# Kernel optimization log

Hardware: AMD Instinct MI355X
Metric: run time of the kernel (lower is better)

## Reference

```python
import jax, jax.numpy as jnp
import numpy as np

B, D, E, H, TOP_K = 8192, 1024, 16, 1024, 8
LOSS_COEF = 0.01
NOISE_EPS = 0.01
INV_SQRT2 = 0.7071067811865476


def _normal_cdf(z):
    return 0.5 * (1.0 + jax.lax.erf(z * INV_SQRT2))


def _cv_squared(v):
    v = v.astype(jnp.float32)
    return jnp.var(v, ddof=1) / (jnp.mean(v) ** 2 + 1e-10)


def setup_inputs() -> dict:
    key = jax.random.key(0)
    k1, k2, k3, k4, k5, k6 = jax.random.split(key, 6)
    return {
        "x": jax.random.normal(k1, (B, D), dtype=jnp.float32),
        "w_gate": jax.random.normal(k2, (D, E), dtype=jnp.float32) * 0.02,
        "w_noise": jax.random.normal(k3, (D, E), dtype=jnp.float32) * 0.02,
        "expert_w": jax.random.normal(k4, (E, D, H), dtype=jnp.float32) * (1.0 / np.sqrt(D)),
        "expert_b": jax.random.normal(k5, (E, H), dtype=jnp.float32) * 0.01,
        "noise": jax.random.normal(k6, (B, E), dtype=jnp.float32),
    }


def reference(x, w_gate, w_noise, expert_w, expert_b, noise):
    # ---- noisy top-k gating (training=True) ----
    clean_logits = x @ w_gate                                   # [B, E]
    raw_noise_stddev = x @ w_noise                              # [B, E]
    noise_stddev = jax.nn.softplus(raw_noise_stddev) + NOISE_EPS
    noisy_logits = clean_logits + noise * noise_stddev          # [B, E]
    probs = jax.nn.softmax(noisy_logits, axis=1)                # [B, E]

    m = min(TOP_K + 1, E)
    top_logits, top_indices = jax.lax.top_k(probs, m)           # [B, m]
    top_k_logits = top_logits[:, :TOP_K]
    top_k_indices = top_indices[:, :TOP_K]
    top_k_gates = top_k_logits / (jnp.sum(top_k_logits, axis=1, keepdims=True) + 1e-6)

    rows = jnp.arange(B)[:, None]
    gates = jnp.zeros_like(probs).at[rows, top_k_indices].set(top_k_gates)  # [B, E]

    # ---- prob-in-top-k load (top_k < num_experts, training) ----
    # faithful to source: thresholds come from softmaxed top values,
    # compared against pre-softmax noisy/clean logits (as in original code)
    threshold_if_in = top_logits[:, TOP_K][:, None]             # [B, 1]
    threshold_if_out = top_logits[:, TOP_K - 1][:, None]        # [B, 1]
    is_in = noisy_logits > threshold_if_in
    prob_if_in = _normal_cdf((clean_logits - threshold_if_in) / noise_stddev)
    prob_if_out = _normal_cdf((clean_logits - threshold_if_out) / noise_stddev)
    load = jnp.where(is_in, prob_if_in, prob_if_out).sum(axis=0)  # [E]

    importance = gates.sum(axis=0)                              # [E]
    loss = LOSS_COEF * (_cv_squared(importance) + _cv_squared(load))

    # ---- experts: per-expert linear, gate-weighted sum over experts ----
    # y[b,h] = sum_e gates[b,e] * (x[b,:] @ W[e] + b[e])[h]
    y = jnp.einsum('bd,edh,be->bh', x, expert_w, gates) + gates @ expert_b
    return y, loss
```

## Files before the change

### kernel.cpp

```cpp
#include <hip/hip_runtime.h>
#include <cstdint>

#define B_SZ 8192
#define D_SZ 1024
#define E_SZ 16
#define H_SZ 1024
#define MAXTILES 272

using short8 = __attribute__((ext_vector_type(8))) short;
using f32x4  = __attribute__((ext_vector_type(4))) float;

__device__ __forceinline__ unsigned short f2bf(float f) {
  union { float f; unsigned int u; } v; v.f = f;
  unsigned int u = v.u;
  return (unsigned short)((u + 0x7fffu + ((u >> 16) & 1u)) >> 16);
}
__device__ __forceinline__ float bf2f(unsigned short h) {
  union { unsigned int u; float f; } v; v.u = ((unsigned int)h) << 16; return v.f;
}

__device__ __forceinline__ void async_ld16(void* lds, const void* g) {
  __builtin_amdgcn_global_load_lds(
      reinterpret_cast<const unsigned int __attribute__((address_space(1)))*>(
          reinterpret_cast<uintptr_t>(g)),
      reinterpret_cast<unsigned int __attribute__((address_space(3)))*>(
          reinterpret_cast<uintptr_t>(lds)),
      16, 0, 0);
}

__global__ __launch_bounds__(256) void prep(
    const float* __restrict__ x, const float* __restrict__ wg,
    const float* __restrict__ wn, const float* __restrict__ ew,
    unsigned short* __restrict__ xb, unsigned short* __restrict__ wtb,
    float* __restrict__ cl, float* __restrict__ rn, float* __restrict__ stats) {
  __shared__ __align__(16) float psm[2 * 32 * 132];
  const int bx = blockIdx.x;
  const int tid = threadIdx.x;

  if (bx < 256) {
    float* sx  = psm;
    float* swT = psm + 32 * 132;
    const int lane = tid & 63;
    const int wave = tid >> 6;
    const int row  = lane & 31;
    const int half = lane >> 5;
    const int rowbase = bx * 32;
    float acc[8] = {0.f, 0.f, 0.f, 0.f, 0.f, 0.f, 0.f, 0.f};

    const int srow = tid >> 3;
    const int sd   = (tid & 7) * 16;
    const int wd   = tid >> 1;
    const int wc   = (tid & 1) * 16;
    const float* wsrc = (wc == 0) ? wg : wn;

    for (int ch = 0; ch < 8; ++ch) {
      __syncthreads();
      #pragma unroll
      for (int k = 0; k < 4; ++k) {
        const float4 v = *(const float4*)(
            x + (size_t)(rowbase + srow) * D_SZ + ch * 128 + sd + k * 4);
        *(float4*)&sx[srow * 132 + sd + k * 4] = v;
      }
      {
        const float* wp = wsrc + (size_t)(ch * 128 + wd) * 16;
        float wv[16];
        #pragma unroll
        for (int k = 0; k < 4; ++k)
          *(float4*)&wv[k * 4] = *(const float4*)(wp + k * 4);
        #pragma unroll
        for (int j = 0; j < 16; ++j) swT[(wc + j) * 132 + wd] = wv[j];
      }
      __syncthreads();
      #pragma unroll 4
      for (int dg = 0; dg < 16; ++dg) {
        const int d = half * 64 + dg * 4;
        const f32x4 xv = *(const f32x4*)&sx[row * 132 + d];
        #pragma unroll
        for (int c = 0; c < 8; ++c) {
          const f32x4 wv = *(const f32x4*)&swT[(wave * 8 + c) * 132 + d];
          acc[c] = fmaf(xv[0], wv[0], acc[c]);
          acc[c] = fmaf(xv[1], wv[1], acc[c]);
          acc[c] = fmaf(xv[2], wv[2], acc[c]);
          acc[c] = fmaf(xv[3], wv[3], acc[c]);
        }
      }
    }
    #pragma unroll
    for (int c = 0; c < 8; ++c) acc[c] += __shfl_down(acc[c], 32);
    if (lane < 32) {
      const int cg = wave * 8;
      float* dst = (cg < 16) ? (cl + (size_t)(rowbase + row) * 16 + cg)
                             : (rn + (size_t)(rowbase + row) * 16 + (cg - 16));
      *(float4*)dst = *(const float4*)&acc[0];
      *(float4*)(dst + 4) = *(const float4*)&acc[4];
    }
  } else if (bx < 4352) {
    const int b = bx - 256;
    const size_t i = (size_t)b * 256 + tid;
    const float4 v0 = ((const float4*)x)[2 * i];
    const float4 v1 = ((const float4*)x)[2 * i + 1];
    unsigned short r[8] = {f2bf(v0.x), f2bf(v0.y), f2bf(v0.z), f2bf(v0.w),
                           f2bf(v1.x), f2bf(v1.y), f2bf(v1.z), f2bf(v1.w)};
    ((short8*)xb)[i] = *(const short8*)r;
    if (b == 0 && tid < 48) stats[tid] = 0.0f;
  } else {
    float (*t)[65] = (float(*)[65])psm;
    const int b = bx - 4352;
    const int e  = b >> 8;
    const int d0 = ((b >> 4) & 15) * 64;
    const int h0 = (b & 15) * 64;
    const float* We = ew + (size_t)e * D_SZ * H_SZ;
    unsigned short* Wte = wtb + (size_t)e * D_SZ * H_SZ;
    #pragma unroll
    for (int i = 0; i < 4; ++i) {
      const int idx = i * 256 + tid;
      const int r = idx >> 4, co = (idx & 15) * 4;
      *(float4*)&t[r][co] =
          *(const float4*)(We + (size_t)(d0 + r) * H_SZ + h0 + co);
    }
    __syncthreads();
    #pragma unroll
    for (int i = 0; i < 2; ++i) {
      const int idx = i * 256 + tid;
      const int r = idx >> 3, c8 = (idx & 7) * 8;
      unsigned short v[8];
      #pragma unroll
      for (int j = 0; j < 8; ++j) v[j] = f2bf(t[c8 + j][r]);
      *(short8*)(Wte + (size_t)(h0 + r) * D_SZ + d0 + c8) = *(const short8*)v;
    }
  }
}

__global__ __launch_bounds__(64) void gating_post(
    const float* __restrict__ clg, const float* __restrict__ rng,
    const float* __restrict__ noise, float* __restrict__ gates,
    float* __restrict__ stats, int* __restrict__ rowidx, int* __restrict__ rowmap) {
  int* gcount = (int*)(stats + 32);
  __shared__ int lcnt[16];
  __shared__ int lbase[16];
  const int row = blockIdx.x * 64 + threadIdx.x;
  if (threadIdx.x < 16) lcnt[threadIdx.x] = 0;
  float cl[16], sd[16], nl[16], p[16];
  #pragma unroll
  for (int e = 0; e < 16; ++e) {
    cl[e] = clg[(size_t)row * 16 + e];
    const float r = rng[(size_t)row * 16 + e];
    sd[e] = fmaxf(r, 0.0f) + log1pf(expf(-fabsf(r))) + 0.01f;
    nl[e] = cl[e] + noise[(size_t)row * 16 + e] * sd[e];
  }
  float mx = nl[0];
  #pragma unroll
  for (int e = 1; e < 16; ++e) mx = fmaxf(mx, nl[e]);
  float sum = 0.0f;
  #pragma unroll
  for (int e = 0; e < 16; ++e) { p[e] = expf(nl[e] - mx); sum += p[e]; }
  const float inv = 1.0f / sum;
  #pragma unroll
  for (int e = 0; e < 16; ++e) p[e] *= inv;
  float tmp[16];
  #pragma unroll
  for (int e = 0; e < 16; ++e) tmp[e] = p[e];
  float tv[9]; int ti[9];
  for (int k = 0; k < 9; ++k) {
    float bv = tmp[0]; int bj = 0;
    #pragma unroll
    for (int j = 1; j < 16; ++j) if (tmp[j] > bv) { bv = tmp[j]; bj = j; }
    tv[k] = bv; ti[k] = bj; tmp[bj] = -1.0f;
  }
  float s8 = 0.0f;
  #pragma unroll
  for (int k = 0; k < 8; ++k) s8 += tv[k];
  const float denom = s8 + 1e-6f;
  float g[16];
  #pragma unroll
  for (int e = 0; e < 16; ++e) g[e] = 0.0f;
  for (int k = 0; k < 8; ++k) g[ti[k]] = tv[k] / denom;
  const float thr_in = tv[8], thr_out = tv[7];
  float lc[16];
  #pragma unroll
  for (int e = 0; e < 16; ++e) {
    const float t = (nl[e] > thr_in) ? thr_in : thr_out;
    lc[e] = 0.5f * (1.0f + erff(((cl[e] - t) / sd[e]) * 0.70710678118654752f));
  }
  #pragma unroll
  for (int e = 0; e < 16; ++e) gates[(size_t)row * 16 + e] = g[e];
  __syncthreads();
  int myslot[8];
  #pragma unroll
  for (int k = 0; k < 8; ++k) myslot[k] = atomicAdd(&lcnt[ti[k]], 1);
  __syncthreads();
  if (threadIdx.x < 16) lbase[threadIdx.x] = atomicAdd(&gcount[threadIdx.x], lcnt[threadIdx.x]);
  __syncthreads();
  #pragma unroll
  for (int k = 0; k < 8; ++k) {
    const int e = ti[k];
    const int slot = lbase[e] + myslot[k];
    rowidx[e * B_SZ + slot] = row;
    rowmap[row * 8 + k] = (e << 13) | slot;
  }
  #pragma unroll
  for (int e = 0; e < 16; ++e) {
    float vi = g[e], vl = lc[e];
    for (int o = 32; o > 0; o >>= 1) { vi += __shfl_down(vi, o); vl += __shfl_down(vl, o); }
    if (threadIdx.x == 0) {
      atomicAdd(&stats[e], vi);
      atomicAdd(&stats[16 + e], vl);
    }
  }
}

__global__ __launch_bounds__(512, 2) void moe_gemm(
    const unsigned short* __restrict__ Xb,
    const unsigned short* __restrict__ Wt,
    const float* __restrict__ gates,
    const float* __restrict__ ebias,
    const float* __restrict__ stats,
    const int* __restrict__ rowidx,
    unsigned short* __restrict__ partial) {
  __shared__ __align__(16) char smem[133120];
  int*   sRI = (int*)(smem + 131072);
  float* sGG = (float*)(smem + 132096);

  const int* gcount = (const int*)(stats + 32);
  int my_e = -1, tile = 0, tstart = 0, acc_t = 0;
  #pragma unroll
  for (int ee = 0; ee < 16; ++ee) {
    const int nt_e = (gcount[ee] + 255) >> 8;
    if (my_e < 0 && (int)blockIdx.y < acc_t + nt_e) {
      my_e = ee; tile = (int)blockIdx.y - acc_t; tstart = acc_t;
    }
    acc_t += nt_e;
  }
  if (my_e < 0) return;
  const int e = my_e;
  const int slot0 = tile << 8;
  const int cnt = gcount[e];
  const int col0 = (int)blockIdx.x << 8;

  const int tid  = (int)threadIdx.x;
  const int lane = tid & 63;
  const int wave = tid >> 6;
  const int wm = wave >> 2, wn = wave & 3;
  const int ml = lane & 15;
  const int quad = lane >> 4;
  const int wb = tid & ~63;

  if (tid < 256) {
    const int slot = slot0 + tid;
    const int ok = slot < cnt;
    const int row = ok ? rowidx[e * B_SZ + slot] : 0;
    sRI[tid] = row;
    sGG[tid] = ok ? gates[(size_t)row * 16 + e] : 0.0f;
  }
  __syncthreads();

  const int gc = (tid & 7) ^ ((tid >> 3) & 7);
  const int rl = tid >> 3;
  const unsigned short* const We = Wt + (size_t)e * D_SZ * H_SZ;
  const unsigned short* a_src0 = Xb + (size_t)sRI[rl]       * D_SZ + gc * 8;
  const unsigned short* a_src1 = Xb + (size_t)sRI[64 + rl]  * D_SZ + gc * 8;
  const unsigned short* a_src2 = Xb + (size_t)sRI[128 + rl] * D_SZ + gc * 8;
  const unsigned short* a_src3 = Xb + (size_t)sRI[192 + rl] * D_SZ + gc * 8;
  const unsigned short* b_src0 = We + (size_t)(col0 + rl)   * D_SZ + gc * 8;

#define STG_A(kt, l) \
  async_ld16(smem + (((kt) & 1) * 32768) + ((((l) * 512 + wb)) << 4), \
             a_src##l + (kt) * 64)
#define STG_B(kt, l) \
  async_ld16(smem + 65536 + (((kt) & 1) * 32768) + ((((l) * 512 + wb)) << 4), \
             b_src0 + (l) * 65536 + (kt) * 64)

  STG_A(0,0); STG_A(0,1);  STG_A(0,2); STG_A(0,3);
  STG_B(0,0); STG_B(0,1);  STG_B(0,2); STG_B(0,3);
  STG_A(1,0); STG_A(1,1);  STG_A(1,2); STG_A(1,3);
  STG_B(1,0); STG_B(1,1);
  asm volatile("s_waitcnt vmcnt(6)" ::: "memory");
  __builtin_amdgcn_s_barrier();

  f32x4 acc[8][4] = {};

#define MF16(I0) \
  do { __builtin_amdgcn_s_setprio(1); \
    _Pragma("unroll") for (int ii = 0; ii < 2; ++ii) \
      _Pragma("unroll") for (int j = 0; j < 4; ++j) \
        _Pragma("unroll") for (int kk = 0; kk < 2; ++kk) \
          acc[(I0)+ii][j] = __builtin_amdgcn_mfma_f32_16x16x32_bf16( \
              af[(I0)+ii][kk], bf[j][kk], acc[(I0)+ii][j], 0, 0, 0); \
    __builtin_amdgcn_s_setprio(0); } while (0)

  #pragma unroll
  for (int kt = 0; kt < 16; ++kt) {
    const unsigned short* sAb =
        (const unsigned short*)(smem + ((kt & 1) ? 32768 : 0));
    const unsigned short* sBb =
        (const unsigned short*)(smem + 65536 + ((kt & 1) ? 32768 : 0));
    if (kt + 1 < 16) { STG_B(kt+1,2); STG_B(kt+1,3); }
    short8 af[8][2], bf[4][2];
    #pragma unroll
    for (int i = 0; i < 8; ++i) {
      const int m = wm * 128 + i * 16 + ml;
      #pragma unroll
      for (int kk = 0; kk < 2; ++kk) {
        const int c = (kk * 4 + quad) ^ (m & 7);
        af[i][kk] = *(const short8*)(sAb + (size_t)(m * 8 + c) * 8);
      }
    }
    #pragma unroll
    for (int j = 0; j < 4; ++j) {
      const int n = wn * 64 + j * 16 + ml;
      #pragma unroll
      for (int kk = 0; kk < 2; ++kk) {
        const int c = (kk * 4 + quad) ^ (n & 7);
        bf[j][kk] = *(const short8*)(sBb + (size_t)(n * 8 + c) * 8);
      }
    }
    MF16(0);
    asm volatile("s_waitcnt lgkmcnt(0)" ::: "memory");
    __builtin_amdgcn_s_barrier();
    if (kt + 2 < 16) { STG_A(kt+2,0); STG_A(kt+2,1); }
    MF16(2);
    if (kt + 2 < 16) { STG_A(kt+2,2); STG_A(kt+2,3); }
    MF16(4);
    if (kt + 2 < 16) { STG_B(kt+2,0); STG_B(kt+2,1); }
    MF16(6);
    if (kt <= 13) {
      asm volatile("s_waitcnt vmcnt(6)" ::: "memory");
      __builtin_amdgcn_s_barrier();
    } else if (kt == 14) {
      asm volatile("s_waitcnt vmcnt(0)" ::: "memory");
      __builtin_amdgcn_s_barrier();
    }
  }
#undef MF16
#undef STG_A
#undef STG_B

  __syncthreads();
  float ebv[4];
  #pragma unroll
  for (int j = 0; j < 4; ++j)
    ebv[j] = ebias[(size_t)e * H_SZ + col0 + wn * 64 + j * 16 + ml];
  unsigned short* sOut = (unsigned short*)smem;
  const size_t prow0 = (size_t)((tstart << 8) + slot0);
  #pragma unroll
  for (int half = 0; half < 2; ++half) {
    if (wm == half) {
      #pragma unroll
      for (int i = 0; i < 8; ++i) {
        const int lr = i * 16 + quad * 4;
        #pragma unroll
        for (int r = 0; r < 4; ++r) {
          const float gv = sGG[half * 128 + lr + r];
          #pragma unroll
          for (int j = 0; j < 4; ++j) {
            const int cc = wn * 64 + j * 16 + ml;
            sOut[(lr + r) * 264 + cc] = f2bf(gv * (acc[i][j][r] + ebv[j]));
          }
        }
      }
    }
    __syncthreads();
    #pragma unroll
    for (int it = 0; it < 8; ++it) {
      const int s = it * 512 + tid;
      const int rr = s >> 5;
      const int c8 = (s & 31) * 8;
      const short8 v = *(const short8*)(sOut + rr * 264 + c8);
      __builtin_nontemporal_store(
          v, (short8*)(partial + (prow0 + half * 128 + rr) * H_SZ + col0 + c8));
    }
    __syncthreads();
  }
}

__global__ __launch_bounds__(256) void reduce_k(
    const unsigned short* __restrict__ partial, const int* __restrict__ rowmap,
    const float* __restrict__ stats, float* __restrict__ y) {
  const int row0 = blockIdx.x * 4;
  const int tid = threadIdx.x;
  const int* gcount = (const int*)(stats + 32);
  __shared__ int sp[4][8];
  if (tid < 32) {
    const int r = tid >> 3, k = tid & 7;
    const int v = rowmap[(row0 + r) * 8 + k];
    const int e = v >> 13, slot = v & 8191;
    int t = 0;
    #pragma unroll
    for (int ee = 0; ee < 16; ++ee) t += (ee < e) ? ((gcount[ee] + 255) >> 8) : 0;
    sp[r][k] = (t << 8) + slot;
  }
  __syncthreads();
  const int r = tid >> 6;
  const int c0 = (tid & 63) * 16;
  float a[16];
  #pragma unroll
  for (int j = 0; j < 16; ++j) a[j] = 0.f;
  #pragma unroll
  for (int k = 0; k < 8; ++k) {
    const unsigned short* pp = partial + (size_t)sp[r][k] * H_SZ + c0;
    const short8 p0 = *(const short8*)pp;
    const short8 p1 = *(const short8*)(pp + 8);
    #pragma unroll
    for (int j = 0; j < 8; ++j) {
      a[j]     += bf2f((unsigned short)p0[j]);
      a[j + 8] += bf2f((unsigned short)p1[j]);
    }
  }
  float* yp = y + (size_t)(row0 + r) * H_SZ + c0;
  #pragma unroll
  for (int q = 0; q < 4; ++q) {
    float4 o = {a[q * 4], a[q * 4 + 1], a[q * 4 + 2], a[q * 4 + 3]};
    *(float4*)(yp + q * 4) = o;
  }

  if (blockIdx.x == 0 && tid == 0) {
    double si = 0.0, sl = 0.0;
    for (int e = 0; e < 16; ++e) { si += stats[e]; sl += stats[16 + e]; }
    const double mi = si / 16.0, mld = sl / 16.0;
    double vi = 0.0, vl = 0.0;
    for (int e = 0; e < 16; ++e) {
      const double di = stats[e] - mi;       vi += di * di;
      const double dl = stats[16 + e] - mld; vl += dl * dl;
    }
    vi /= 15.0; vl /= 15.0;
    const double loss = 0.01 * (vi / (mi * mi + 1e-10) + vl / (mld * mld + 1e-10));
    y[(size_t)B_SZ * H_SZ] = (float)loss;
  }
}

extern "C" void kernel_launch(void* const* d_in, const int* in_sizes, int n_in,
                              void* d_out, int out_size, void* d_ws, size_t ws_size,
                              hipStream_t stream) {
  (void)in_sizes; (void)n_in; (void)out_size; (void)ws_size;
  const float* x    = (const float*)d_in[0];
  const float* wg   = (const float*)d_in[1];
  const float* wnoi = (const float*)d_in[2];
  const float* ew   = (const float*)d_in[3];
  const float* eb   = (const float*)d_in[4];
  const float* nz   = (const float*)d_in[5];
  float* y = (float*)d_out;

  char* ws = (char*)d_ws;
  const size_t MB = 1024 * 1024;
  unsigned short* xb     = (unsigned short*)(ws);
  unsigned short* wtb    = (unsigned short*)(ws + 16 * MB);
  float* cl              = (float*)(ws + 48 * MB);
  float* rn              = (float*)(ws + 48 * MB + 512 * 1024);
  float* gates           = (float*)(ws + 49 * MB);
  int*   rowidx          = (int*)  (ws + 49 * MB + 512 * 1024);
  int*   rowmap          = (int*)  (ws + 50 * MB);
  float* stats           = (float*)(ws + 50 * MB + 512 * 1024);
  unsigned short* partial= (unsigned short*)(ws + 52 * MB);

  hipLaunchKernelGGL(prep,        dim3(8448),         dim3(256), 0, stream,
                     x, wg, wnoi, ew, xb, wtb, cl, rn, stats);
  hipLaunchKernelGGL(gating_post, dim3(128),          dim3(64),  0, stream,
                     cl, rn, nz, gates, stats, rowidx, rowmap);
  hipLaunchKernelGGL(moe_gemm,    dim3(4, MAXTILES),  dim3(512), 0, stream,
                     xb, wtb, gates, eb, stats, rowidx, partial);
  hipLaunchKernelGGL(reduce_k,    dim3(2048),         dim3(256), 0, stream,
                     partial, rowmap, stats, y);
}
```

Baseline: 391.3 us.

## Interleave per-phase LDS reads with MFMA blocks and reorder async staging

Restructures the main K-loop of the expert GEMM into four phases. Each phase reads only a 2-row slice of A fragments from LDS, then waits and runs its MFMA block, rather than loading all A fragments up front. Global-to-LDS staging is reordered so that the A halves for the next tile and the B halves for tile+2 are issued between phases. The aim is to cut register pressure and overlap LDS reads with MFMAs, at the cost of many more barriers per iteration. The stage ordering also changes which buffers the vmcnt(6) waits cover, so correctness depends on the new issue order lining up with the waits.

```diff
diff --git a/kernel.cpp b/kernel.cpp
--- a/kernel.cpp
+++ b/kernel.cpp
@@ -270,22 +270,43 @@
   async_ld16(smem + 65536 + (((kt) & 1) * 32768) + ((((l) * 512 + wb)) << 4), \
              b_src0 + (l) * 65536 + (kt) * 64)
 
-  STG_A(0,0); STG_A(0,1);  STG_A(0,2); STG_A(0,3);
-  STG_B(0,0); STG_B(0,1);  STG_B(0,2); STG_B(0,3);
-  STG_A(1,0); STG_A(1,1);  STG_A(1,2); STG_A(1,3);
-  STG_B(1,0); STG_B(1,1);
+  STG_A(0,0); STG_A(0,2);
+  STG_B(0,0); STG_B(0,1); STG_B(0,2); STG_B(0,3);
+  STG_A(0,1); STG_A(0,3);
+  STG_A(1,0); STG_A(1,2);
+  STG_B(1,0); STG_B(1,1); STG_B(1,2); STG_B(1,3);
   asm volatile("s_waitcnt vmcnt(6)" ::: "memory");
   __builtin_amdgcn_s_barrier();
 
   f32x4 acc[8][4] = {};
 
-#define MF16(I0) \
+#define RD_B() \
+  do { _Pragma("unroll") for (int j = 0; j < 4; ++j) { \
+    const int n = wn * 64 + j * 16 + ml; \
+    _Pragma("unroll") for (int kk = 0; kk < 2; ++kk) { \
+      const int c = (kk * 4 + quad) ^ (n & 7); \
+      bf[j][kk] = *(const short8*)(sBb + (size_t)(n * 8 + c) * 8); \
+    } } } while (0)
+
+#define RD_A(p) \
+  do { _Pragma("unroll") for (int ii = 0; ii < 2; ++ii) { \
+    const int m = wm * 128 + ((p) * 2 + ii) * 16 + ml; \
+    _Pragma("unroll") for (int kk = 0; kk < 2; ++kk) { \
+      const int c = (kk * 4 + quad) ^ (m & 7); \
+      af[ii][kk] = *(const short8*)(sAb + (size_t)(m * 8 + c) * 8); \
+    } } } while (0)
+
+#define WAIT_LGKM0() \
+  do { asm volatile("s_waitcnt lgkmcnt(0)" ::: "memory"); \
+       __builtin_amdgcn_sched_barrier(0); } while (0)
+
+#define MFP(p) \
   do { __builtin_amdgcn_s_setprio(1); \
     _Pragma("unroll") for (int ii = 0; ii < 2; ++ii) \
       _Pragma("unroll") for (int j = 0; j < 4; ++j) \
         _Pragma("unroll") for (int kk = 0; kk < 2; ++kk) \
-          acc[(I0)+ii][j] = __builtin_amdgcn_mfma_f32_16x16x32_bf16( \
-              af[(I0)+ii][kk], bf[j][kk], acc[(I0)+ii][j], 0, 0, 0); \
+          acc[(p) * 2 + ii][j] = __builtin_amdgcn_mfma_f32_16x16x32_bf16( \
+              af[ii][kk], bf[j][kk], acc[(p) * 2 + ii][j], 0, 0, 0); \
     __builtin_amdgcn_s_setprio(0); } while (0)
 
   #pragma unroll
@@ -294,44 +315,41 @@
         (const unsigned short*)(smem + ((kt & 1) ? 32768 : 0));
     const unsigned short* sBb =
         (const unsigned short*)(smem + 65536 + ((kt & 1) ? 32768 : 0));
-    if (kt + 1 < 16) { STG_B(kt+1,2); STG_B(kt+1,3); }
-    short8 af[8][2], bf[4][2];
-    #pragma unroll
-    for (int i = 0; i < 8; ++i) {
-      const int m = wm * 128 + i * 16 + ml;
-      #pragma unroll
-      for (int kk = 0; kk < 2; ++kk) {
-        const int c = (kk * 4 + quad) ^ (m & 7);
-        af[i][kk] = *(const short8*)(sAb + (size_t)(m * 8 + c) * 8);
-      }
-    }
-    #pragma unroll
-    for (int j = 0; j < 4; ++j) {
-      const int n = wn * 64 + j * 16 + ml;
-      #pragma unroll
-      for (int kk = 0; kk < 2; ++kk) {
-        const int c = (kk * 4 + quad) ^ (n & 7);
-        bf[j][kk] = *(const short8*)(sBb + (size_t)(n * 8 + c) * 8);
-      }
-    }
-    MF16(0);
-    asm volatile("s_waitcnt lgkmcnt(0)" ::: "memory");
-    __builtin_amdgcn_s_barrier();
-    if (kt + 2 < 16) { STG_A(kt+2,0); STG_A(kt+2,1); }
-    MF16(2);
-    if (kt + 2 < 16) { STG_A(kt+2,2); STG_A(kt+2,3); }
-    MF16(4);
-    if (kt + 2 < 16) { STG_B(kt+2,0); STG_B(kt+2,1); }
-    MF16(6);
+    short8 af[2][2], bf[4][2];
+    if (kt + 1 < 16) { STG_A(kt + 1, 1); STG_A(kt + 1, 3); }
+    RD_A(0); RD_B();
+    __builtin_amdgcn_s_barrier();
+    WAIT_LGKM0();
+    MFP(0);
+    __builtin_amdgcn_s_barrier();
+    if (kt + 2 < 16) { STG_B(kt + 2, 0); STG_B(kt + 2, 1); }
+    RD_A(1);
+    __builtin_amdgcn_s_barrier();
+    WAIT_LGKM0();
+    MFP(1);
+    __builtin_amdgcn_s_barrier();
+    if (kt + 2 < 16) { STG_B(kt + 2, 2); STG_B(kt + 2, 3); }
+    RD_A(2);
+    __builtin_amdgcn_s_barrier();
+    WAIT_LGKM0();
+    MFP(2);
+    __builtin_amdgcn_s_barrier();
+    if (kt + 2 < 16) { STG_A(kt + 2, 0); STG_A(kt + 2, 2); }
+    RD_A(3);
+    __builtin_amdgcn_s_barrier();
+    WAIT_LGKM0();
+    MFP(3);
     if (kt <= 13) {
       asm volatile("s_waitcnt vmcnt(6)" ::: "memory");
-      __builtin_amdgcn_s_barrier();
     } else if (kt == 14) {
       asm volatile("s_waitcnt vmcnt(0)" ::: "memory");
-      __builtin_amdgcn_s_barrier();
-    }
-  }
-#undef MF16
+    }
+    __builtin_amdgcn_s_barrier();
+  }
+#undef MFP
+#undef WAIT_LGKM0
+#undef RD_A
+#undef RD_B
 #undef STG_A
 #undef STG_B
 
```

Result: no change. 392.5 us (+0.3%).
